# Optimization experiments

Hardware: AMD Instinct MI355X
Metric: run time of the kernel (lower is better)

## Reference

```python
import jax, jax.numpy as jnp
import numpy as np

N = 100000      # nodes
E = 1600000     # edges (before self-loops)
F_IN = 256      # input features
H = 8           # heads, layer 1
FH = 8          # features per head, layer 1
C = 64          # n_classes (layer 2 out, heads=1)
SLOPE = 0.2     # leaky relu negative slope


def setup_inputs() -> dict:
    key = jax.random.key(0)
    ks = jax.random.split(key, 12)
    x = jax.random.normal(ks[0], (N, F_IN), jnp.float32)
    edge_index = jax.random.randint(ks[1], (2, E), 0, N, dtype=jnp.int32)
    # scalar edge weights in [0.5, 1.5) so the (1 - 1/w) correction is well-behaved
    edge_weight = jax.random.uniform(ks[2], (E,), jnp.float32, 0.5, 1.5)
    W1 = jax.random.normal(ks[3], (F_IN, H * FH), jnp.float32) / np.sqrt(F_IN)
    att_src1 = jax.random.normal(ks[4], (H, FH), jnp.float32) * 0.1
    att_dst1 = jax.random.normal(ks[5], (H, FH), jnp.float32) * 0.1
    b1 = jnp.zeros((H * FH,), jnp.float32)
    W2 = jax.random.normal(ks[6], (H * FH, C), jnp.float32) / np.sqrt(H * FH)
    att_src2 = jax.random.normal(ks[7], (1, C), jnp.float32) * 0.1
    att_dst2 = jax.random.normal(ks[8], (1, C), jnp.float32) * 0.1
    b2 = jnp.zeros((C,), jnp.float32)
    return {"x": x, "edge_index": edge_index, "edge_weight": edge_weight,
            "W1": W1, "att_src1": att_src1, "att_dst1": att_dst1, "b1": b1,
            "W2": W2, "att_src2": att_src2, "att_dst2": att_dst2, "b2": b2}


def _gat_layer(x, src, dst, ew, W, a_src, a_dst, b, heads, fph, concat):
    n = x.shape[0]
    h = (x @ W).reshape(n, heads, fph)                      # [N,H,F]
    al_src = jnp.sum(h * a_src, axis=-1)                    # [N,H]
    al_dst = jnp.sum(h * a_dst, axis=-1)                    # [N,H]
    alpha = jax.nn.leaky_relu(al_src[src] + al_dst[dst], SLOPE)  # [E,H]
    alpha = alpha + (1.0 - 1.0 / ew)[:, None]               # scalar edge-weight correction
    # segment softmax over destination nodes
    m = jax.ops.segment_max(alpha, dst, num_segments=n)
    e = jnp.exp(alpha - m[dst])
    s = jax.ops.segment_sum(e, dst, num_segments=n)
    alpha = e / (s[dst] + 1e-16)                            # [E,H]
    msg = h[src] * alpha[:, :, None]                        # [E,H,F]
    out = jax.ops.segment_sum(msg, dst, num_segments=n)     # [N,H,F]
    out = out.reshape(n, heads * fph) if concat else out.mean(axis=1)
    return out + b


def reference(x, edge_index, edge_weight, W1, att_src1, att_dst1, b1,
              W2, att_src2, att_dst2, b2):
    n = x.shape[0]
    loops = jnp.arange(n, dtype=edge_index.dtype)
    src = jnp.concatenate([edge_index[0], loops])
    dst = jnp.concatenate([edge_index[1], loops])
    ew = jnp.concatenate([edge_weight, jnp.ones((n,), edge_weight.dtype)])  # fill_value=1.0
    # dropout layers are identity in eval mode
    h = _gat_layer(x, src, dst, ew, W1, att_src1, att_dst1, b1, H, FH, concat=True)
    h = jax.nn.elu(h)
    out = _gat_layer(h, src, dst, ew, W2, att_src2, att_dst2, b2, 1, C, concat=False)
    return out
```

## Files before the change

### kernel.cpp

```cpp
#include <hip/hip_runtime.h>
#include <math.h>

#define NNODES 100000
#define NEDGES 1600000
#define EATOT  1700000
#define FIN    256
#define C1     64
#define NH     8
#define C2     64
#define SLOPE  0.2f
#define LOG2E  1.4426950408889634f
#define QSCALE 8192.0f

#define NBKT  391
#define BCAP  5120
#define EPB_A 4096
#define NBLK_A 416

#define NT1 3125
#define NT2 1563
#define GGRID 512

typedef __attribute__((ext_vector_type(8))) short short8;
typedef __attribute__((ext_vector_type(4))) float f32x4;

__device__ __forceinline__ unsigned short f2bf(float f){
  unsigned u = __float_as_uint(f);
  unsigned r = (u + 0x7FFFu + ((u >> 16) & 1u)) >> 16;
  return (unsigned short)r;
}

__device__ __forceinline__ void splitw_body(const float* __restrict__ W,
                                            short* __restrict__ th, short* __restrict__ tl,
                                            int K, int idx){
  int k = idx >> 6, c = idx & 63;
  float w = W[idx];
  unsigned int b = __float_as_uint(w);
  unsigned short h = (unsigned short)(b >> 16);
  float hf = __uint_as_float(b & 0xffff0000u);
  float rem = w - hf;
  unsigned short lo = (unsigned short)(__float_as_uint(rem) >> 16);
  th[c * K + k] = (short)h;
  tl[c * K + k] = (short)lo;
}

__global__ void k_pre(const float* __restrict__ W1, short* __restrict__ w1h,
                      short* __restrict__ w1l, const float* __restrict__ W2,
                      short* __restrict__ w2h, short* __restrict__ w2l,
                      int* __restrict__ gcount){
  int b = blockIdx.x, t = threadIdx.x;
  if (b < 64){
    splitw_body(W1, w1h, w1l, FIN, b * 256 + t);
  } else if (b < 80){
    splitw_body(W2, w2h, w2l, C1, (b - 64) * 256 + t);
  } else {
    for (int i = t; i < NBKT; i += 256) gcount[i] = 0;
  }
}

__global__ __launch_bounds__(256) void k_bucketA(
    const int* __restrict__ ei, const float* __restrict__ ew,
    int* __restrict__ gcount, uint2* __restrict__ brec){
  __shared__ int cnt[NBKT];
  __shared__ int base[NBKT];
  int t = threadIdx.x;
  for (int i = t; i < NBKT; i += 256) cnt[i] = 0;
  __syncthreads();
  int e0 = blockIdx.x * EPB_A;
  int e1 = e0 + EPB_A; if (e1 > EATOT) e1 = EATOT;

  int dv[16]; unsigned pv[16];
  #pragma unroll
  for (int i = 0; i < 16; ++i){
    int e = e0 + t + i * 256;
    dv[i] = -1;
    if (e < e1){
      int s, d; float corr;
      if (e < NEDGES){ s = ei[e]; d = ei[NEDGES + e]; corr = 1.0f - 1.0f / ew[e]; }
      else { s = e - NEDGES; d = s; corr = 0.0f; }
      int q = __float2int_rn(corr * (LOG2E * QSCALE));
      dv[i] = d;
      pv[i] = ((unsigned)q << 17) | (unsigned)s;
      atomicAdd(&cnt[d >> 8], 1);
    }
  }
  __syncthreads();
  for (int i = t; i < NBKT; i += 256){
    int c = cnt[i];
    base[i] = c ? atomicAdd(&gcount[i], c) : 0;
    cnt[i] = 0;
  }
  __syncthreads();
  #pragma unroll
  for (int i = 0; i < 16; ++i){
    if (dv[i] >= 0){
      int bkt = dv[i] >> 8;
      int rel = base[bkt] + atomicAdd(&cnt[bkt], 1);
      brec[(size_t)bkt * BCAP + rel] = make_uint2((unsigned)dv[i], pv[i]);
    }
  }
}

__global__ void k_bucketS(const int* __restrict__ gcount, int* __restrict__ gbase,
                          int* __restrict__ rowptr){
  __shared__ int sh[512];
  int t = threadIdx.x;
  int v = (t < NBKT) ? gcount[t] : 0;
  sh[t] = v; __syncthreads();
  for (int off = 1; off < 512; off <<= 1){
    int y = (t >= off) ? sh[t - off] : 0;
    __syncthreads();
    sh[t] += y;
    __syncthreads();
  }
  if (t < NBKT) gbase[t] = sh[t] - v;
  if (t == 0) rowptr[NNODES] = EATOT;
}

__global__ __launch_bounds__(256, 2) void k_bg1(
    const uint2* __restrict__ brec, const int* __restrict__ gcount,
    const int* __restrict__ gbase, int* __restrict__ rowptr, int* __restrict__ rec,
    const float* __restrict__ X, const short* __restrict__ Bth,
    const short* __restrict__ Btl, const float* __restrict__ asrc,
    const float* __restrict__ adst, unsigned short* __restrict__ Hout,
    float* __restrict__ alsrc, float* __restrict__ aldst)
{
  __shared__ float xbuf[2][32 * 256];

  if (blockIdx.x < NBKT){
    int* hist  = (int*)&xbuf[0][0];
    int* scanb = hist + 256;
    int* excl  = scanb + 256;
    int* cur   = excl + 256;
    int bkt = blockIdx.x;
    int t = threadIdx.x;
    int n0 = bkt << 8;
    int cnt = gcount[bkt];
    int gb = gbase[bkt];
    hist[t] = 0;
    __syncthreads();
    const uint2* breg = brec + (size_t)bkt * BCAP;
    for (int j = t; j < cnt; j += 256)
      atomicAdd(&hist[breg[j].x & 255u], 1);
    __syncthreads();
    int h = hist[t];
    scanb[t] = h;
    __syncthreads();
    for (int off = 1; off < 256; off <<= 1){
      int y = (t >= off) ? scanb[t - off] : 0;
      __syncthreads();
      scanb[t] += y;
      __syncthreads();
    }
    int ex = scanb[t] - h;
    excl[t] = ex;
    cur[t] = 0;
    if (n0 + t < NNODES) rowptr[n0 + t] = gb + ex;
    __syncthreads();
    for (int j = t; j < cnt; j += 256){
      uint2 r = breg[j];
      int dl = (int)(r.x & 255u);
      int pos = gb + excl[dl] + atomicAdd(&cur[dl], 1);
      rec[pos] = (int)r.y;
    }
    return;
  }

  const int lane = threadIdx.x & 63;
  const int wave = threadIdx.x >> 6;
  const int l15 = lane & 15;
  const int kg = lane >> 4;
  const int cp = wave & 1;
  const int rh = wave >> 1;
  const int rl = rh * 16 + l15;
  const int rs = rl & 7;

  short8 bh[8][2], bl[8][2];
  #pragma unroll
  for (int ks = 0; ks < 8; ++ks){
    #pragma unroll
    for (int cc = 0; cc < 2; ++cc){
      unsigned boff = (unsigned)((cp * 2 + cc) * 16 + l15) * FIN + ks * 32 + kg * 8;
      bh[ks][cc] = *(const short8*)&Bth[boff];
      bl[ks][cc] = *(const short8*)&Btl[boff];
    }
  }
  float ascv[2], adcv[2];
  #pragma unroll
  for (int cc = 0; cc < 2; ++cc){
    ascv[cc] = asrc[(cp * 2 + cc) * 16 + l15] * LOG2E;
    adcv[cc] = adst[(cp * 2 + cc) * 16 + l15] * LOG2E;
  }

  const int t0 = blockIdx.x - NBKT;
  #pragma unroll
  for (int t = 0; t < 8; ++t){
    int r = wave * 8 + t;
    unsigned u = (unsigned)(lane ^ (r & 7));
    __builtin_amdgcn_global_load_lds(
        (const unsigned int*)(X + (size_t)(t0 * 32 + r) * FIN + u * 4),
        (unsigned int*)&xbuf[0][r * 256], 16, 0, 0);
  }

  int cur = 0;
  for (int ti = t0; ti < NT1; ti += GGRID){
    __syncthreads();
    int nxt = ti + GGRID;
    if (nxt < NT1){
      #pragma unroll
      for (int t = 0; t < 8; ++t){
        int r = wave * 8 + t;
        unsigned u = (unsigned)(lane ^ (r & 7));
        __builtin_amdgcn_global_load_lds(
            (const unsigned int*)(X + (size_t)(nxt * 32 + r) * FIN + u * 4),
            (unsigned int*)&xbuf[cur ^ 1][r * 256], 16, 0, 0);
      }
    }

    f32x4 acc[2] = {f32x4{0,0,0,0}, f32x4{0,0,0,0}};
    #pragma unroll
    for (int ks = 0; ks < 8; ++ks){
      int k0 = ks * 32 + kg * 8;
      unsigned U = (unsigned)(k0 >> 2);
      float4 xa = *(const float4*)&xbuf[cur][rl * 256 + ((U ^ rs) << 2)];
      float4 xb = *(const float4*)&xbuf[cur][rl * 256 + (((U + 1) ^ rs) << 2)];
      float xs[8] = {xa.x, xa.y, xa.z, xa.w, xb.x, xb.y, xb.z, xb.w};
      short8 ah, al;
      #pragma unroll
      for (int j = 0; j < 8; ++j){
        unsigned u = __float_as_uint(xs[j]);
        ah[j] = (short)(u >> 16);
        float hf = __uint_as_float(u & 0xffff0000u);
        al[j] = (short)(__float_as_uint(xs[j] - hf) >> 16);
      }
      #pragma unroll
      for (int cc = 0; cc < 2; ++cc){
        acc[cc] = __builtin_amdgcn_mfma_f32_16x16x32_bf16(ah, bh[ks][cc], acc[cc], 0, 0, 0);
        acc[cc] = __builtin_amdgcn_mfma_f32_16x16x32_bf16(ah, bl[ks][cc], acc[cc], 0, 0, 0);
        acc[cc] = __builtin_amdgcn_mfma_f32_16x16x32_bf16(al, bh[ks][cc], acc[cc], 0, 0, 0);
      }
    }

    int rowg = ti * 32 + rh * 16 + kg * 4;
    #pragma unroll
    for (int cc = 0; cc < 2; ++cc){
      #pragma unroll
      for (int reg = 0; reg < 4; ++reg)
        Hout[(size_t)(rowg + reg) * 64 + (cp * 2 + cc) * 16 + l15] = f2bf(acc[cc][reg]);
    }
    #pragma unroll
    for (int reg = 0; reg < 4; ++reg){
      int r = rowg + reg;
      #pragma unroll
      for (int cc = 0; cc < 2; ++cc){
        float ps = acc[cc][reg] * ascv[cc];
        float pd = acc[cc][reg] * adcv[cc];
        ps += __shfl_xor(ps, 1, 64); ps += __shfl_xor(ps, 2, 64); ps += __shfl_xor(ps, 4, 64);
        pd += __shfl_xor(pd, 1, 64); pd += __shfl_xor(pd, 2, 64); pd += __shfl_xor(pd, 4, 64);
        if ((l15 & 7) == 0){
          int head = (cp * 2 + cc) * 2 + (l15 >> 3);
          alsrc[r * NH + head] = ps;
          aldst[r * NH + head] = pd;
        }
      }
    }
    cur ^= 1;
  }
}

__global__ __launch_bounds__(256, 2) void k_gemm2(
    const unsigned short* __restrict__ Ah, const unsigned short* __restrict__ Al,
    const short* __restrict__ Bth, const short* __restrict__ Btl,
    const float* __restrict__ asrc, const float* __restrict__ adst,
    unsigned short* __restrict__ Hout, float* __restrict__ alsrc,
    float* __restrict__ aldst)
{
  __shared__ unsigned short abuf[2][2][64 * 64];
  const int lane = threadIdx.x & 63;
  const int wave = threadIdx.x >> 6;
  const int l15 = lane & 15;
  const int kg = lane >> 4;
  const int rl = wave * 16 + l15;
  const int rs = rl & 7;

  short8 bh[2][4], bl[2][4];
  #pragma unroll
  for (int ks = 0; ks < 2; ++ks){
    #pragma unroll
    for (int c = 0; c < 4; ++c){
      unsigned boff = (unsigned)(c * 16 + l15) * C1 + ks * 32 + kg * 8;
      bh[ks][c] = *(const short8*)&Bth[boff];
      bl[ks][c] = *(const short8*)&Btl[boff];
    }
  }
  float ascv[4], adcv[4];
  #pragma unroll
  for (int c = 0; c < 4; ++c){
    ascv[c] = asrc[c * 16 + l15] * LOG2E;
    adcv[c] = adst[c * 16 + l15] * LOG2E;
  }

  const int t0 = blockIdx.x;
  auto stage = [&](int buf, int tile){
    #pragma unroll
    for (int j = 0; j < 4; ++j){
      int q = wave * 4 + j;
      int p = q >> 3, rb = q & 7;
      int r = rb * 8 + (lane >> 3);
      int rg = tile * 64 + r; if (rg > NNODES - 1) rg = NNODES - 1;
      unsigned u = (unsigned)((lane & 7) ^ (lane >> 3));
      const unsigned short* src = (p ? Al : Ah) + (size_t)rg * 64 + u * 8;
      __builtin_amdgcn_global_load_lds(
          (const unsigned int*)src,
          (unsigned int*)&abuf[buf][p][rb * 512], 16, 0, 0);
    }
  };
  stage(0, t0);

  int cur = 0;
  for (int ti = t0; ti < NT2; ti += GGRID){
    __syncthreads();
    int nxt = ti + GGRID;
    if (nxt < NT2) stage(cur ^ 1, nxt);

    f32x4 acc[4] = {f32x4{0,0,0,0}, f32x4{0,0,0,0}, f32x4{0,0,0,0}, f32x4{0,0,0,0}};
    #pragma unroll
    for (int ks = 0; ks < 2; ++ks){
      unsigned U = (unsigned)(ks * 4 + kg);
      short8 ah = *(const short8*)&abuf[cur][0][rl * 64 + ((U ^ rs) << 3)];
      short8 al = *(const short8*)&abuf[cur][1][rl * 64 + ((U ^ rs) << 3)];
      #pragma unroll
      for (int c = 0; c < 4; ++c){
        acc[c] = __builtin_amdgcn_mfma_f32_16x16x32_bf16(ah, bh[ks][c], acc[c], 0, 0, 0);
        acc[c] = __builtin_amdgcn_mfma_f32_16x16x32_bf16(ah, bl[ks][c], acc[c], 0, 0, 0);
        acc[c] = __builtin_amdgcn_mfma_f32_16x16x32_bf16(al, bh[ks][c], acc[c], 0, 0, 0);
      }
    }

    int rowg = ti * 64 + wave * 16 + kg * 4;
    #pragma unroll
    for (int c = 0; c < 4; ++c){
      #pragma unroll
      for (int reg = 0; reg < 4; ++reg){
        int r = rowg + reg;
        if (r < NNODES) Hout[(size_t)r * 64 + c * 16 + l15] = f2bf(acc[c][reg]);
      }
    }
    #pragma unroll
    for (int reg = 0; reg < 4; ++reg){
      int r = rowg + reg;
      float ps = 0.0f, pd = 0.0f;
      #pragma unroll
      for (int c = 0; c < 4; ++c){
        ps = fmaf(acc[c][reg], ascv[c], ps);
        pd = fmaf(acc[c][reg], adcv[c], pd);
      }
      ps += __shfl_xor(ps, 1, 64); ps += __shfl_xor(ps, 2, 64);
      ps += __shfl_xor(ps, 4, 64); ps += __shfl_xor(ps, 8, 64);
      pd += __shfl_xor(pd, 1, 64); pd += __shfl_xor(pd, 2, 64);
      pd += __shfl_xor(pd, 4, 64); pd += __shfl_xor(pd, 8, 64);
      if (l15 == 0 && r < NNODES){ alsrc[r] = ps; aldst[r] = pd; }
    }
    cur ^= 1;
  }
}

template<int HEADS, bool DO_ELU, bool SPLIT_OUT>
__global__ __launch_bounds__(256) void k_agg(
    const int* __restrict__ rec, const int* __restrict__ rowptr,
    const unsigned short* __restrict__ hbuf,
    const float* __restrict__ alsrc, const float* __restrict__ aldst,
    const float* __restrict__ bias, float* __restrict__ outF,
    unsigned short* __restrict__ outH, unsigned short* __restrict__ outL){
  int tid = blockIdx.x * blockDim.x + threadIdx.x;
  int d = tid >> 6;
  int c = threadIdx.x & 63;
  if (d >= NNODES) return;
  d = __builtin_amdgcn_readfirstlane(d);
  int beg = rowptr[d], end = rowptr[d + 1];
  int h = (HEADS == 8) ? (c >> 3) : 0;
  float ad = aldst[(size_t)d * HEADS + h];
  float s = 0.0f, acc = 0.0f;

  auto body = [&](int w, float a, float hv){
    float v = a + ad;
    v = fmaxf(v, v * SLOPE);
    v += (float)(w >> 17) * (1.0f / QSCALE);
    v = fminf(v, 60.0f);
    float e = __builtin_amdgcn_exp2f(v);
    s += e;
    acc = fmaf(e, hv, acc);
  };

  int j = beg;
  for (; j + 8 <= end; j += 8){
    int w[8]; float a[8], hv[8];
    #pragma unroll
    for (int i = 0; i < 8; ++i) w[i] = rec[j + i];
    #pragma unroll
    for (int i = 0; i < 8; ++i){
      unsigned si = (unsigned)w[i] & 0x1FFFFu;
      a[i] = alsrc[si * HEADS + h];
      hv[i] = __uint_as_float((unsigned)hbuf[si * 64 + c] << 16);
    }
    #pragma unroll
    for (int i = 0; i < 8; ++i) body(w[i], a[i], hv[i]);
  }
  for (; j < end; ++j){
    int w = rec[j];
    unsigned sj = (unsigned)w & 0x1FFFFu;
    float a = alsrc[sj * HEADS + h];
    float hv = __uint_as_float((unsigned)hbuf[sj * 64 + c] << 16);
    body(w, a, hv);
  }

  float o = acc / (s + 1e-16f) + bias[c];
  if (DO_ELU) o = (o > 0.0f) ? o : (__expf(o) - 1.0f);
  if (SPLIT_OUT){
    unsigned u = __float_as_uint(o);
    outH[(size_t)d * 64 + c] = (unsigned short)(u >> 16);
    float hf = __uint_as_float(u & 0xffff0000u);
    outL[(size_t)d * 64 + c] = (unsigned short)(__float_as_uint(o - hf) >> 16);
  } else {
    outF[(size_t)d * 64 + c] = o;
  }
}

extern "C" void kernel_launch(void* const* d_in, const int* in_sizes, int n_in,
                              void* d_out, int out_size, void* d_ws, size_t ws_size,
                              hipStream_t stream) {
  const float* x    = (const float*)d_in[0];
  const int*   ei   = (const int*)d_in[1];
  const float* ew   = (const float*)d_in[2];
  const float* W1   = (const float*)d_in[3];
  const float* as1  = (const float*)d_in[4];
  const float* ad1  = (const float*)d_in[5];
  const float* b1   = (const float*)d_in[6];
  const float* W2   = (const float*)d_in[7];
  const float* as2  = (const float*)d_in[8];
  const float* ad2  = (const float*)d_in[9];
  const float* b2   = (const float*)d_in[10];
  float* dout = (float*)d_out;

  float* ws = (float*)d_ws;
  size_t off = 0;
  auto alloc = [&](size_t nfloats) -> float* {
    float* p = ws + off;
    off += (nfloats + 15) & ~(size_t)15;
    return p;
  };
  unsigned short* h1 = (unsigned short*)alloc((size_t)NNODES * C1 / 2);
  unsigned short* o1h = (unsigned short*)alloc((size_t)NNODES * C1 / 2);
  unsigned short* o1l = (unsigned short*)alloc((size_t)NNODES * C1 / 2);
  float* alsrc1  = alloc((size_t)NNODES * NH);
  float* aldst1  = alloc((size_t)NNODES * NH);
  float* alsrc2  = alloc(NNODES);
  float* aldst2  = alloc(NNODES);
  int*   gcount  = (int*)alloc(NBKT + 16);
  int*   gbase   = (int*)alloc(NBKT + 16);
  int*   rowptr  = (int*)alloc(NNODES + 1);
  int*   rec     = (int*)alloc(EATOT);
  uint2* brec    = (uint2*)alloc((size_t)NBKT * BCAP * 2);
  short* wt1h    = (short*)alloc(64 * FIN / 2);
  short* wt1l    = (short*)alloc(64 * FIN / 2);
  short* wt2h    = (short*)alloc(64 * C1 / 2);
  short* wt2l    = (short*)alloc(64 * C1 / 2);
  unsigned short* h2 = h1;

  const int BS = 256;

  hipLaunchKernelGGL(k_pre, dim3(81), dim3(BS), 0, stream,
                     W1, wt1h, wt1l, W2, wt2h, wt2l, gcount);

  hipLaunchKernelGGL(k_bucketA, dim3(NBLK_A), dim3(BS), 0, stream, ei, ew, gcount, brec);
  hipLaunchKernelGGL(k_bucketS, dim3(1), dim3(512), 0, stream, gcount, gbase, rowptr);

  hipLaunchKernelGGL(k_bg1, dim3(NBKT + GGRID), dim3(BS), 0, stream,
                     brec, gcount, gbase, rowptr, rec,
                     x, wt1h, wt1l, as1, ad1, h1, alsrc1, aldst1);

  int agrid = (NNODES * 64 + BS - 1) / BS;

  hipLaunchKernelGGL((k_agg<NH, true, true>), dim3(agrid), dim3(BS), 0, stream,
                     rec, rowptr, h1, alsrc1, aldst1, b1, (float*)nullptr, o1h, o1l);

  hipLaunchKernelGGL(k_gemm2, dim3(GGRID), dim3(BS), 0, stream,
                     o1h, o1l, wt2h, wt2l, as2, ad2, h2, alsrc2, aldst2);
  hipLaunchKernelGGL((k_agg<1, false, false>), dim3(agrid), dim3(BS), 0, stream,
                     rec, rowptr, h2, alsrc2, aldst2, b2, dout,
                     (unsigned short*)nullptr, (unsigned short*)nullptr);
}
```

Before: 212.9 us.

## Compute edge attention weights once per edge cooperatively, share via LDS in aggregation

The aggregation kernel previously had every lane recompute the leaky-relu/exp attention score for every edge, which is redundant across the 64 channel lanes. Now each lane computes the score for a different edge (one per head-edge pair for 8 heads, one edge per lane for 1 head) and stores the exp weight plus a precomputed byte offset of the source row in LDS. The lanes then read these back and gather the feature values. This removes redundant rec/alsrc loads and exp work but adds LDS traffic and relies on implicit wavefront-synchronous LDS visibility without barriers.

```diff
diff --git a/kernel.cpp b/kernel.cpp
--- a/kernel.cpp
+++ b/kernel.cpp
@@ -372,46 +372,56 @@
     const float* __restrict__ alsrc, const float* __restrict__ aldst,
     const float* __restrict__ bias, float* __restrict__ outF,
     unsigned short* __restrict__ outH, unsigned short* __restrict__ outL){
+  __shared__ uint2 wLds[4][64];
   int tid = blockIdx.x * blockDim.x + threadIdx.x;
-  int d = tid >> 6;
-  int c = threadIdx.x & 63;
-  if (d >= NNODES) return;
-  d = __builtin_amdgcn_readfirstlane(d);
+  int dn = tid >> 6;
+  int lane = threadIdx.x & 63;
+  int w4 = (threadIdx.x >> 6) & 3;
+  if (dn >= NNODES) return;
+  int d = __builtin_amdgcn_readfirstlane(dn);
   int beg = rowptr[d], end = rowptr[d + 1];
-  int h = (HEADS == 8) ? (c >> 3) : 0;
-  float ad = aldst[(size_t)d * HEADS + h];
+  const int c = lane;
+  const int hc = (HEADS == 8) ? (c >> 3) : 0;
+  const int eslot = (HEADS == 8) ? (lane >> 3) : lane;
+  const int hw = (HEADS == 8) ? (lane & 7) : 0;
+  const int CHUNK = (HEADS == 8) ? 8 : 64;
+  const unsigned cOff = (unsigned)c * 2;
+  float ad_w = aldst[(size_t)d * HEADS + hw];
   float s = 0.0f, acc = 0.0f;
 
-  auto body = [&](int w, float a, float hv){
-    float v = a + ad;
+  for (int j0 = beg; j0 < end; j0 += CHUNK){
+    int je = j0 + eslot;
+    bool valid = (je < end);
+    int w = rec[valid ? je : (end - 1)];
+    unsigned src = (unsigned)w & 0x1FFFFu;
+    float a = alsrc[src * HEADS + hw];
+    float v = a + ad_w;
     v = fmaxf(v, v * SLOPE);
     v += (float)(w >> 17) * (1.0f / QSCALE);
     v = fminf(v, 60.0f);
-    float e = __builtin_amdgcn_exp2f(v);
-    s += e;
-    acc = fmaf(e, hv, acc);
-  };
-
-  int j = beg;
-  for (; j + 8 <= end; j += 8){
-    int w[8]; float a[8], hv[8];
-    #pragma unroll
-    for (int i = 0; i < 8; ++i) w[i] = rec[j + i];
-    #pragma unroll
-    for (int i = 0; i < 8; ++i){
-      unsigned si = (unsigned)w[i] & 0x1FFFFu;
-      a[i] = alsrc[si * HEADS + h];
-      hv[i] = __uint_as_float((unsigned)hbuf[si * 64 + c] << 16);
-    }
-    #pragma unroll
-    for (int i = 0; i < 8; ++i) body(w[i], a[i], hv[i]);
-  }
-  for (; j < end; ++j){
-    int w = rec[j];
-    unsigned sj = (unsigned)w & 0x1FFFFu;
-    float a = alsrc[sj * HEADS + h];
-    float hv = __uint_as_float((unsigned)hbuf[sj * 64 + c] << 16);
-    body(w, a, hv);
+    float e = valid ? __builtin_amdgcn_exp2f(v) : 0.0f;
+    wLds[w4][lane] = make_uint2(__float_as_uint(e), src << 7);
+
+    int rem = end - j0;
+    int n8 = (HEADS == 8) ? 8 : ((rem >= 64) ? 64 : ((rem + 7) & ~7));
+    for (int i0 = 0; i0 < n8; i0 += 8){
+      uint2 wv[8];
+      #pragma unroll
+      for (int i = 0; i < 8; ++i)
+        wv[i] = wLds[w4][(HEADS == 8) ? (i * 8 + hc) : (i0 + i)];
+      float hv[8];
+      #pragma unroll
+      for (int i = 0; i < 8; ++i){
+        unsigned short raw = *(const unsigned short*)((const char*)hbuf + wv[i].y + cOff);
+        hv[i] = __uint_as_float((unsigned)raw << 16);
+      }
+      #pragma unroll
+      for (int i = 0; i < 8; ++i){
+        float ev = __uint_as_float(wv[i].x);
+        s += ev;
+        acc = fmaf(ev, hv[i], acc);
+      }
+    }
   }
 
   float o = acc / (s + 1e-16f) + bias[c];
```

Measured after the change: 193.2 us, median of 2. 1.1x faster.
